# Optimization experiments

Hardware: AMD Instinct MI355X
Metric: run time of the kernel (lower is better)

The kernel has to match this reference:

```python
import jax, jax.numpy as jnp
import numpy as np

# ---- static config (matches init_kwargs) ----
B, N, DIM = 1, 2048, 1024
H, KVH, D = 16, 8, 64
GQ = H // KVH                 # grouped queries per kv head
WS = 64                       # sliding window size (causal, exact)
CBS, STRIDE = 32, 16          # compress block size / sliding stride
SEL_BLK, NSEL, NMEM = 32, 4, 1
NCB = N // STRIDE             # num compressed blocks (128)
NFB = N // SEL_BLK            # num fine blocks (64)
NCPF = SEL_BLK // STRIDE      # compressed blocks per fine block (2)
HID = CBS * D                 # compress MLP hidden (expand factor 1.0)
SCALE = D ** -0.5
THETA = 10000.0
NEG = -jnp.finfo(jnp.float32).max


def setup_inputs():
    key = jax.random.key(0)
    ks = jax.random.split(key, 16)
    s = 0.02
    r = lambda i, shape: jax.random.normal(ks[i], shape, jnp.float32) * s
    return {
        "inp": jax.random.normal(ks[0], (B, N, DIM), jnp.float32),
        "norm_g": jnp.ones((DIM,), jnp.float32),
        "Wqkv": r(1, (DIM, (H + 2 * KVH) * D)),
        "mem_kv": r(2, (2, KVH, NMEM, D)),
        "k_pos": r(3, (KVH, CBS, D)),
        "v_pos": r(4, (KVH, CBS, D)),
        "kW1": r(5, (CBS * D, HID)), "kb1": jnp.zeros((HID,), jnp.float32),
        "kW2": r(6, (HID, D)), "kb2": jnp.zeros((D,), jnp.float32),
        "vW1": r(7, (CBS * D, HID)), "vb1": jnp.zeros((HID,), jnp.float32),
        "vW2": r(8, (HID, D)), "vb2": jnp.zeros((D,), jnp.float32),
        "combW": r(9, (DIM, 3 * H)),
        "combB": jnp.tile(jnp.array([-2.0, -2.0, 2.0], jnp.float32), H),
        "Wout": r(10, (H * D, DIM)),
    }


def _rope(t):
    # lucidrains rotary-embedding-torch: interleaved adjacent-pair rotation
    inv_freq = 1.0 / (THETA ** (jnp.arange(0, D, 2, dtype=jnp.float32) / D))
    ang = jnp.arange(N, dtype=jnp.float32)[:, None] * inv_freq        # [N, D/2]
    cos = jnp.repeat(jnp.cos(ang), 2, axis=-1)                        # [N, D]
    sin = jnp.repeat(jnp.sin(ang), 2, axis=-1)
    t2 = t.reshape(*t.shape[:-1], D // 2, 2)
    rot = jnp.stack([-t2[..., 1], t2[..., 0]], axis=-1).reshape(t.shape)
    return t * cos + rot * sin


def _forward(inp, norm_g, Wqkv, mem_kv, k_pos, v_pos,
             kW1, kb1, kW2, kb2, vW1, vb1, vW2, vb2,
             combW, combB, Wout):
    # RMSNorm
    x = inp * jax.lax.rsqrt(jnp.mean(inp * inp, -1, keepdims=True)
                            + jnp.finfo(inp.dtype).eps) * norm_g
    qkv = x @ Wqkv
    q, k, v = jnp.split(qkv, [H * D, H * D + KVH * D], axis=-1)
    q = q.reshape(B, N, H, D).transpose(0, 2, 1, 3)      # b h n d
    k = k.reshape(B, N, KVH, D).transpose(0, 2, 1, 3)    # b kvh n d
    v = v.reshape(B, N, KVH, D).transpose(0, 2, 1, 3)

    # ---- compressed branch (overlapping windows, left zero pad) ----
    overlap = CBS - STRIDE
    kp = jnp.pad(k, ((0, 0), (0, 0), (overlap, 0), (0, 0)))
    vp = jnp.pad(v, ((0, 0), (0, 0), (overlap, 0), (0, 0)))
    widx = jnp.arange(NCB)[:, None] * STRIDE + jnp.arange(CBS)[None, :]  # [NCB, CBS]
    kw = kp[:, :, widx] + k_pos[None, :, None]   # b kvh w cbs d
    vw = vp[:, :, widx] + v_pos[None, :, None]

    def cmlp(t, W1, b1, W2, b2):
        t = t.reshape(B, KVH, NCB, CBS * D)
        return jax.nn.relu(t @ W1 + b1) @ W2 + b2       # b kvh w d

    ck = cmlp(kw, kW1, kb1, kW2, kb2)
    cv = cmlp(vw, vW1, vb1, vW2, vb2)
    ck = jnp.concatenate([jnp.broadcast_to(mem_kv[0], (B, KVH, NMEM, D)), ck], 2)
    cv = jnp.concatenate([jnp.broadcast_to(mem_kv[1], (B, KVH, NMEM, D)), cv], 2)

    qg = q.reshape(B, KVH, GQ, N, D)
    csim = jnp.einsum('bhgid,bhjd->bhgij', qg, ck) * SCALE   # no mask (cmask=None)
    cattn = jax.nn.softmax(csim, -1)
    cout = jnp.einsum('bhgij,bhjd->bhgid', cattn, cv).reshape(B, H, N, D)

    # rotary AFTER compressed attention (as in source)
    rq, rk = _rope(q), _rope(k)

    # ---- importance scores -> top-k fine block selection ----
    imp = csim[..., NMEM:].mean(2)                          # b kvh n NCB (share grouped q)
    imp = imp.reshape(B, KVH, N, NFB, NCPF).mean(-1)        # mean-pool to fine blocks
    q_blk = jnp.arange(N) // SEL_BLK
    diag = q_blk[:, None] == jnp.arange(NFB)[None, :]
    imp = jnp.where(diag[None, None], NEG, imp)             # mask own (diagonal) block
    imp = jax.nn.softmax(jnp.pad(imp, ((0, 0),) * 3 + ((1, 0),),
                                 constant_values=-1000.0), -1)[..., 1:]
    sel_val, sel_idx = jax.lax.top_k(imp, NSEL)             # b kvh n NSEL

    # ---- fine (block-selected) attention ----
    own = jnp.broadcast_to(q_blk[None, None, :, None], (B, KVH, N, 1))
    sel_idx = jnp.concatenate([sel_idx, own], -1)           # append own block
    fmask = jnp.repeat((sel_val > 1e-10)[..., None], SEL_BLK, -1)  # b kvh n NSEL blk
    causal_row = jnp.tril(jnp.ones((SEL_BLK, SEL_BLK), bool))[jnp.arange(N) % SEL_BLK]
    causal = jnp.broadcast_to(causal_row[None, None, :, None, :],
                              (B, KVH, N, 1, SEL_BLK))
    fmask = jnp.concatenate([fmask, causal], 3).reshape(B, KVH, N, (NSEL + 1) * SEL_BLK)

    fk_blocks = rk.reshape(B, KVH, NFB, SEL_BLK, D)
    fv_blocks = v.reshape(B, KVH, NFB, SEL_BLK, D)
    gather = jax.vmap(jax.vmap(lambda blocks, idx: blocks[idx]))  # over b, kvh
    fk = gather(fk_blocks, sel_idx).reshape(B, KVH, N, (NSEL + 1) * SEL_BLK, D)
    fv = gather(fv_blocks, sel_idx).reshape(B, KVH, N, (NSEL + 1) * SEL_BLK, D)

    rqg = rq.reshape(B, KVH, GQ, N, D)
    fsim = jnp.einsum('bhgid,bhijd->bhgij', rqg, fk) * SCALE
    fsim = jnp.where(fmask[:, :, None], fsim, NEG / 10)
    fattn = jax.nn.softmax(fsim, -1)
    fout = jnp.einsum('bhgij,bhijd->bhgid', fattn, fv).reshape(B, H, N, D)

    # ---- sliding window (causal, exact window size WS) ----
    NW = N // WS
    kp2 = jnp.pad(rk, ((0, 0), (0, 0), (WS, 0), (0, 0)))
    vp2 = jnp.pad(v, ((0, 0), (0, 0), (WS, 0), (0, 0)))
    kidx = jnp.arange(NW)[:, None] * WS + jnp.arange(2 * WS)[None, :]
    kwin = kp2[:, :, kidx]                                  # b kvh nw 2ws d
    vwin = vp2[:, :, kidx]
    qwin = rqg.reshape(B, KVH, GQ, NW, WS, D)
    ssim = jnp.einsum('bhgwid,bhwjd->bhgwij', qwin, kwin) * SCALE
    i = jnp.arange(WS)[:, None]
    j = jnp.arange(2 * WS)[None, :]
    diff = i - (j - WS)
    local_ok = (diff >= 0) & (diff < WS)                    # [WS, 2WS]
    keypos = jnp.arange(NW)[:, None, None] * WS + (jnp.arange(2 * WS) - WS)[None, None, :]
    smask = local_ok[None] & (keypos >= 0)                  # [NW, WS, 2WS]
    ssim = jnp.where(smask[None, None, None], ssim, NEG)
    sattn = jax.nn.softmax(ssim, -1)
    sout = jnp.einsum('bhgwij,bhwjd->bhgwid', sattn, vwin).reshape(B, H, N, D)

    # ---- learned strategy combination (compressed, fine, sliding) ----
    gates = jax.nn.sigmoid(x @ combW + combB).reshape(B, N, H, 3).transpose(0, 2, 1, 3)
    out = gates[..., 0:1] * cout + gates[..., 1:2] * fout + gates[..., 2:3] * sout
    out = out.transpose(0, 2, 1, 3).reshape(B, N, H * D) @ Wout
    return out


def reference(inp, norm_g, Wqkv, mem_kv, k_pos, v_pos,
              kW1, kb1, kW2, kb2, vW1, vb1, vW2, vb2,
              combW, combB, Wout):
    return _forward(inp, norm_g, Wqkv, mem_kv, k_pos, v_pos,
                    kW1, kb1, kW2, kb2, vW1, vb1, vW2, vb2,
                    combW, combB, Wout)
```

## Files before the change

kernel.cpp:

```cpp
#include <hip/hip_runtime.h>
#include <hip/hip_bf16.h>

#define NTOK 2048
#define DIM 1024
#define NH 16
#define KVH 8
#define GQ 2
#define HD 64
#define WS 64
#define CBS 32
#define STRIDE 16
#define SEL_BLK 32
#define NSEL 4
#define NMEM 1
#define NCB 128
#define NFB 64
#define HIDN 2048
#define SCALE 0.125f
#define NEGF (-3.4028234663852886e38f)
#define NEG10F (-3.4028234663852886e37f)

typedef __attribute__((ext_vector_type(8))) short bf16x8;
typedef __attribute__((ext_vector_type(4))) float f32x4;

__device__ __forceinline__ float bflo(unsigned u) { return __uint_as_float(u << 16); }
__device__ __forceinline__ float bfhi(unsigned u) { return __uint_as_float(u & 0xffff0000u); }
__device__ __forceinline__ void dot8(const float4& qa, const float4& qb, uint4 a, float& s) {
    s += qa.x * bflo(a.x) + qa.y * bfhi(a.x) + qa.z * bflo(a.y) + qa.w * bfhi(a.y) +
         qb.x * bflo(a.z) + qb.y * bfhi(a.z) + qb.z * bflo(a.w) + qb.w * bfhi(a.w);
}

__device__ __forceinline__ void gload_lds16(const void* g, void* l) {
    __builtin_amdgcn_global_load_lds((const __attribute__((address_space(1))) unsigned*)g,
                                     (__attribute__((address_space(3))) unsigned*)l, 16, 0, 0);
}

__device__ __forceinline__ void rms_body(const float* __restrict__ inp,
                                         const float* __restrict__ g,
                                         float* __restrict__ x,
                                         __hip_bfloat16* __restrict__ xb, int n) {
    const float* row = inp + (size_t)n * DIM;
    float ss = 0.f;
    for (int c = threadIdx.x; c < DIM; c += 256) { float v = row[c]; ss += v * v; }
    __shared__ float red[4];
    for (int o = 32; o; o >>= 1) ss += __shfl_down(ss, o, 64);
    if ((threadIdx.x & 63) == 0) red[threadIdx.x >> 6] = ss;
    __syncthreads();
    if (threadIdx.x == 0) red[0] = red[0] + red[1] + red[2] + red[3];
    __syncthreads();
    float rs = 1.0f / sqrtf(red[0] / (float)DIM + 1.1920928955078125e-07f);
    float* xr = x + (size_t)n * DIM;
    __hip_bfloat16* xbr = xb + (size_t)n * DIM;
    for (int c = threadIdx.x; c < DIM; c += 256) {
        float v = row[c] * rs * g[c];
        xr[c] = v;
        xbr[c] = __float2bfloat16(v);
    }
}

__device__ __forceinline__ void transpose_body(const float* __restrict__ B,
                                               __hip_bfloat16* __restrict__ Bt,
                                               int K, int N, int bx, int by) {
    __shared__ float tile[32][33];
    int n0 = bx * 32, k0 = by * 32;
    int x = threadIdx.x & 31, y = threadIdx.x >> 5;
    for (int i = 0; i < 4; i++) {
        int k = k0 + y + 8 * i, n = n0 + x;
        tile[y + 8 * i][x] = (k < K && n < N) ? B[(size_t)k * N + n] : 0.f;
    }
    __syncthreads();
    for (int i = 0; i < 4; i++) {
        int n = n0 + y + 8 * i, k = k0 + x;
        if (n < N && k < K) Bt[(size_t)n * K + k] = __float2bfloat16(tile[x][y + 8 * i]);
    }
}

__global__ __launch_bounds__(256) void pre_kernel(
    const float* inp, const float* norm_g, float* x, __hip_bfloat16* xb,
    const float* Wqkv, __hip_bfloat16* Wqkvt,
    const float* kW1, __hip_bfloat16* kW1t,
    const float* vW1, __hip_bfloat16* vW1t,
    const float* Wout, __hip_bfloat16* Woutt,
    const float* combW, __hip_bfloat16* combWt,
    const float* kW2, __hip_bfloat16* kW2t,
    const float* vW2, __hip_bfloat16* vW2t,
    const float* combB, float* gatesb,
    const float* kb2, float* ckraw,
    const float* vb2, float* cvraw) {
    int b = blockIdx.x;
    if (b < 2048) { rms_body(inp, norm_g, x, xb, b); return; }
    b -= 2048;
    if (b < 2048) { transpose_body(Wqkv, Wqkvt, 1024, 2048, b % 64, b / 64); return; }
    b -= 2048;
    if (b < 4096) { transpose_body(kW1, kW1t, 2048, 2048, b % 64, b / 64); return; }
    b -= 4096;
    if (b < 4096) { transpose_body(vW1, vW1t, 2048, 2048, b % 64, b / 64); return; }
    b -= 4096;
    if (b < 1024) { transpose_body(Wout, Woutt, 1024, 1024, b % 32, b / 32); return; }
    b -= 1024;
    if (b < 64) { transpose_body(combW, combWt, 1024, 48, b % 2, b / 2); return; }
    b -= 64;
    if (b < 128) { transpose_body(kW2, kW2t, 2048, 64, b % 2, b / 2); return; }
    b -= 128;
    if (b < 128) { transpose_body(vW2, vW2t, 2048, 64, b % 2, b / 2); return; }
    b -= 128;
    if (b < 384) {
        int idx = b * 256 + threadIdx.x;
        if (idx < 2048 * 48) gatesb[idx] = combB[idx % 48];
        return;
    }
    b -= 384;
    {
        int idx = b * 256 + threadIdx.x;
        int tot = 1024 * 64;
        if (idx < tot) ckraw[idx] = kb2[idx % 64];
        else if (idx < 2 * tot) { idx -= tot; cvraw[idx] = vb2[idx % 64]; }
        return;
    }
}
#define PRE_BLOCKS (2048 + 2048 + 4096 + 4096 + 1024 + 64 + 128 + 128 + 384 + 512)

template <int ACT, int OUTBF16>
__device__ __forceinline__ void mfma_gemm_body(const __hip_bfloat16* __restrict__ A,
                                               const __hip_bfloat16* __restrict__ Bt,
                                               const float* __restrict__ bias,
                                               void* __restrict__ Cp,
                                               int M, int N, int K, int bx, int by) {
    __shared__ __align__(16) short As[128 * 32];
    __shared__ __align__(16) short Bs[128 * 32];
    int tid = threadIdx.x;
    int lane = tid & 63, wave = tid >> 6;
    int wm = (wave >> 1) * 64, wn = (wave & 1) * 64;
    int m0 = by * 128, n0 = bx * 128;
    f32x4 acc[4][4];
    for (int r = 0; r < 4; r++)
        for (int c = 0; c < 4; c++)
            acc[r][c] = (f32x4){0.f, 0.f, 0.f, 0.f};

    int r0 = tid >> 2, kc0 = (tid & 3) * 8;
    int r1 = r0 + 64;

    for (int k0 = 0; k0 < K; k0 += 32) {
        __syncthreads();
        gload_lds16(A + (size_t)(m0 + r0) * K + k0 + kc0, &As[r0 * 32 + kc0]);
        gload_lds16(A + (size_t)(m0 + r1) * K + k0 + kc0, &As[r1 * 32 + kc0]);
        gload_lds16(Bt + (size_t)(n0 + r0) * K + k0 + kc0, &Bs[r0 * 32 + kc0]);
        gload_lds16(Bt + (size_t)(n0 + r1) * K + k0 + kc0, &Bs[r1 * 32 + kc0]);
        __syncthreads();
        bf16x8 af[4], bfr[4];
#pragma unroll
        for (int r = 0; r < 4; r++)
            af[r] = *(const bf16x8*)&As[(wm + r * 16 + (lane & 15)) * 32 + (lane >> 4) * 8];
#pragma unroll
        for (int c = 0; c < 4; c++)
            bfr[c] = *(const bf16x8*)&Bs[(wn + c * 16 + (lane & 15)) * 32 + (lane >> 4) * 8];
#pragma unroll
        for (int r = 0; r < 4; r++)
#pragma unroll
            for (int c = 0; c < 4; c++)
                acc[r][c] = __builtin_amdgcn_mfma_f32_16x16x32_bf16(af[r], bfr[c], acc[r][c], 0, 0, 0);
    }
    for (int r = 0; r < 4; r++) {
        int grow = m0 + wm + r * 16 + (lane >> 4) * 4;
        for (int c = 0; c < 4; c++) {
            int gcol = n0 + wn + c * 16 + (lane & 15);
            float bv = bias ? bias[gcol] : 0.f;
#pragma unroll
            for (int v = 0; v < 4; v++) {
                float val = acc[r][c][v] + bv;
                if (ACT == 1) val = fmaxf(val, 0.f);
                if (OUTBF16)
                    ((__hip_bfloat16*)Cp)[(size_t)(grow + v) * N + gcol] = __float2bfloat16(val);
                else
                    ((float*)Cp)[(size_t)(grow + v) * N + gcol] = val;
            }
        }
    }
}

template <int ACT, int OUTBF16>
__global__ __launch_bounds__(256) void mfma_gemm(const __hip_bfloat16* __restrict__ A,
                                                 const __hip_bfloat16* __restrict__ Bt,
                                                 const float* __restrict__ bias,
                                                 void* __restrict__ Cp,
                                                 int M, int N, int K) {
    mfma_gemm_body<ACT, OUTBF16>(A, Bt, bias, Cp, M, N, K, blockIdx.x, blockIdx.y);
}

__global__ __launch_bounds__(256) void mfma_gemm_pair(const __hip_bfloat16* A0,
                                                      const __hip_bfloat16* A1,
                                                      const __hip_bfloat16* Bt0,
                                                      const __hip_bfloat16* Bt1,
                                                      const float* bias0, const float* bias1,
                                                      __hip_bfloat16* C0, __hip_bfloat16* C1,
                                                      int M, int N, int K) {
    if (blockIdx.z == 0)
        mfma_gemm_body<1, 1>(A0, Bt0, bias0, C0, M, N, K, blockIdx.x, blockIdx.y);
    else
        mfma_gemm_body<1, 1>(A1, Bt1, bias1, C1, M, N, K, blockIdx.x, blockIdx.y);
}

__device__ __forceinline__ void skgemm_body(const __hip_bfloat16* __restrict__ A,
                                            const __hip_bfloat16* __restrict__ Bt,
                                            float* __restrict__ C,
                                            int M, int Nout, int K, int by, int bz, int nz) {
    __shared__ __align__(16) short As2[128 * 32];
    __shared__ __align__(16) short Bs2[64 * 32];
    int tid = threadIdx.x;
    int lane = tid & 63, wave = tid >> 6;
    int m0 = by * 128;
    int wm = wave * 32;
    int kchunk = K / nz;
    int kbase = bz * kchunk;
    f32x4 acc[2][4];
    for (int r = 0; r < 2; r++)
        for (int c = 0; c < 4; c++) acc[r][c] = (f32x4){0.f, 0.f, 0.f, 0.f};

    int ra = tid >> 2, kc = (tid & 3) * 8;
    int rb = ra < Nout ? ra : Nout - 1;
    for (int k0 = kbase; k0 < kbase + kchunk; k0 += 32) {
        __syncthreads();
        gload_lds16(A + (size_t)(m0 + ra) * K + k0 + kc, &As2[ra * 32 + kc]);
        gload_lds16(A + (size_t)(m0 + ra + 64) * K + k0 + kc, &As2[(ra + 64) * 32 + kc]);
        gload_lds16(Bt + (size_t)rb * K + k0 + kc, &Bs2[ra * 32 + kc]);
        __syncthreads();
        bf16x8 af[2], bfr[4];
#pragma unroll
        for (int r = 0; r < 2; r++)
            af[r] = *(const bf16x8*)&As2[(wm + r * 16 + (lane & 15)) * 32 + (lane >> 4) * 8];
#pragma unroll
        for (int c = 0; c < 4; c++)
            bfr[c] = *(const bf16x8*)&Bs2[(c * 16 + (lane & 15)) * 32 + (lane >> 4) * 8];
#pragma unroll
        for (int r = 0; r < 2; r++)
#pragma unroll
            for (int c = 0; c < 4; c++)
                acc[r][c] = __builtin_amdgcn_mfma_f32_16x16x32_bf16(af[r], bfr[c], acc[r][c], 0, 0, 0);
    }
    for (int r = 0; r < 2; r++) {
        int grow = m0 + wm + r * 16 + (lane >> 4) * 4;
        for (int c = 0; c < 4; c++) {
            int gcol = c * 16 + (lane & 15);
            if (gcol >= Nout) continue;
#pragma unroll
            for (int v = 0; v < 4; v++)
                atomicAdd(&C[(size_t)(grow + v) * Nout + gcol], acc[r][c][v]);
        }
    }
}

__global__ __launch_bounds__(256) void qkv_gates_kernel(const __hip_bfloat16* xb,
                                                        const __hip_bfloat16* Wqkvt,
                                                        float* qkv,
                                                        const __hip_bfloat16* combWt,
                                                        float* gatesb) {
    int b = blockIdx.x;
    if (b < 256) {
        mfma_gemm_body<0, 0>(xb, Wqkvt, nullptr, qkv, 2048, 2048, 1024, b & 15, b >> 4);
    } else {
        int s = b - 256;
        skgemm_body(xb, combWt, gatesb, 2048, 48, 1024, s & 15, s >> 4, 4);
    }
}

__global__ __launch_bounds__(256) void skgemm_pair(const __hip_bfloat16* A0,
                                                   const __hip_bfloat16* A1,
                                                   const __hip_bfloat16* Bt0,
                                                   const __hip_bfloat16* Bt1,
                                                   float* C0, float* C1,
                                                   int M, int Nout, int K) {
    if (blockIdx.x == 0)
        skgemm_body(A0, Bt0, C0, M, Nout, K, blockIdx.y, blockIdx.z, gridDim.z);
    else
        skgemm_body(A1, Bt1, C1, M, Nout, K, blockIdx.y, blockIdx.z, gridDim.z);
}

__global__ __launch_bounds__(256) void winrope_kernel(const float* __restrict__ qkv,
                                                      const float* __restrict__ k_pos,
                                                      const float* __restrict__ v_pos,
                                                      __hip_bfloat16* __restrict__ kwflat,
                                                      __hip_bfloat16* __restrict__ vwflat,
                                                      float* __restrict__ rq,
                                                      __hip_bfloat16* __restrict__ rk,
                                                      __hip_bfloat16* __restrict__ vt) {
    int b = blockIdx.x;
    int t = threadIdx.x;
    if (b < 4096) {
        size_t total = (size_t)(KVH * NCB) * HIDN;
        for (size_t e = (size_t)b * 256 + t; e < total; e += (size_t)4096 * 256) {
            int r = (int)(e >> 11);
            int c = (int)(e & 2047);
            int j = c >> 6, d = c & 63;
            int h = r >> 7, i = r & 127;
            int p = i * STRIDE + j - (CBS - STRIDE);
            float kb = k_pos[((size_t)h * CBS + j) * HD + d];
            float vb = v_pos[((size_t)h * CBS + j) * HD + d];
            float kv = 0.f, vv = 0.f;
            if (p >= 0) {
                kv = qkv[(size_t)p * 2048 + 1024 + h * HD + d];
                vv = qkv[(size_t)p * 2048 + 1536 + h * HD + d];
            }
            kwflat[e] = __float2bfloat16(kv + kb);
            vwflat[e] = __float2bfloat16(vv + vb);
        }
        return;
    }
    int n = b - 4096;
    for (int idx = t; idx < NH * 32; idx += 256) {
        int h = idx >> 5, f = idx & 31;
        float inv = exp2f((float)f * -0.41524101186092f);
        float ang = (float)n * inv;
        float cc = cosf(ang), ssn = sinf(ang);
        float a = qkv[(size_t)n * 2048 + h * HD + 2 * f];
        float bq = qkv[(size_t)n * 2048 + h * HD + 2 * f + 1];
        float* o = rq + ((size_t)h * NTOK + n) * HD + 2 * f;
        o[0] = a * cc - bq * ssn;
        o[1] = bq * cc + a * ssn;
    }
    for (int idx = t; idx < KVH * 32; idx += 256) {
        int h = idx >> 5, f = idx & 31;
        float inv = exp2f((float)f * -0.41524101186092f);
        float ang = (float)n * inv;
        float cc = cosf(ang), ssn = sinf(ang);
        float a = qkv[(size_t)n * 2048 + 1024 + h * HD + 2 * f];
        float bq = qkv[(size_t)n * 2048 + 1024 + h * HD + 2 * f + 1];
        __hip_bfloat16* o = rk + ((size_t)h * NTOK + n) * HD + 2 * f;
        o[0] = __float2bfloat16(a * cc - bq * ssn);
        o[1] = __float2bfloat16(bq * cc + a * ssn);
    }
    for (int idx = t; idx < KVH * HD; idx += 256) {
        int h = idx >> 6, d = idx & 63;
        vt[((size_t)h * NTOK + n) * HD + d] =
            __float2bfloat16(qkv[(size_t)n * 2048 + 1536 + h * HD + d]);
    }
}

__global__ __launch_bounds__(256) void cattn2_kernel(const float* __restrict__ qkv,
                                                     const float* __restrict__ ckraw,
                                                     const float* __restrict__ cvraw,
                                                     const float* __restrict__ memkv,
                                                     float* __restrict__ cout,
                                                     int* __restrict__ selidx,
                                                     int* __restrict__ selmask) {
    int h = blockIdx.x >> 6;
    int i0 = (blockIdx.x & 63) * 32;
    int t = threadIdx.x;
    __shared__ float qs[64][68];
    __shared__ float sc[64][132];
    __shared__ float scratch[32 * 68];
    __shared__ float memk[64], memv[64];

    for (int idx = t; idx < 4096; idx += 256) {
        int row = idx >> 6, d = idx & 63;
        int g = row >> 5, qi = row & 31;
        qs[row][d] = qkv[(size_t)(i0 + qi) * 2048 + (h * 2 + g) * 64 + d];
    }
    if (t < 64) { memk[t] = memkv[h * 64 + t]; memv[t] = memkv[(8 + h) * 64 + t]; }
    __syncthreads();
    if (t < 64) {
        float s = 0.f;
        for (int d = 0; d < 64; d++) s += qs[t][d] * memk[d];
        sc[t][0] = s * SCALE;
    }
    int rg = t >> 3, kg = t & 7;
    for (int c = 0; c < 4; c++) {
        __syncthreads();
        for (int idx = t; idx < 2048; idx += 256) {
            int jj = idx >> 6, d = idx & 63;
            scratch[jj * 68 + d] = ckraw[((size_t)h * 128 + c * 32 + jj) * 64 + d];
        }
        __syncthreads();
        float a0[4] = {}, a1[4] = {};
        for (int d = 0; d < 64; d += 4) {
            float4 q0 = *(const float4*)&qs[rg * 2][d];
            float4 q1 = *(const float4*)&qs[rg * 2 + 1][d];
#pragma unroll
            for (int kk = 0; kk < 4; kk++) {
                float4 kv = *(const float4*)&scratch[(kg + kk * 8) * 68 + d];
                a0[kk] += q0.x * kv.x + q0.y * kv.y + q0.z * kv.z + q0.w * kv.w;
                a1[kk] += q1.x * kv.x + q1.y * kv.y + q1.z * kv.z + q1.w * kv.w;
            }
        }
#pragma unroll
        for (int kk = 0; kk < 4; kk++) {
            sc[rg * 2][1 + c * 32 + kg + kk * 8] = a0[kk] * SCALE;
            sc[rg * 2 + 1][1 + c * 32 + kg + kk * 8] = a1[kk] * SCALE;
        }
    }
    __syncthreads();
    for (int idx = t; idx < 2048; idx += 256) {
        int qi = idx >> 6, fb = idx & 63;
        float v = 0.25f * (sc[qi][1 + 2 * fb] + sc[qi][2 + 2 * fb] +
                           sc[32 + qi][1 + 2 * fb] + sc[32 + qi][2 + 2 * fb]);
        if (fb == ((i0 + qi) >> 5)) v = NEGF;
        scratch[qi * 66 + fb] = v;
    }
    __syncthreads();
    if (t < 32) {
        float* row = &scratch[t * 66];
        float m = -1000.f;
        for (int j = 0; j < 64; j++) m = fmaxf(m, row[j]);
        float den = __expf(-1000.f - m);
        for (int j = 0; j < 64; j++) den += __expf(row[j] - m);
        float invd = 1.f / den;
        unsigned long long taken = 0ull;
        int mk = 0;
        size_t base = ((size_t)h * NTOK + i0 + t) * 5;
        for (int p = 0; p < NSEL; p++) {
            float bv = NEGF;
            int bi = 0;
            for (int j = 0; j < 64; j++) {
                if (!((taken >> j) & 1ull) && row[j] > bv) { bv = row[j]; bi = j; }
            }
            taken |= 1ull << bi;
            selidx[base + p] = bi;
            if (__expf(bv - m) * invd > 1e-10f) mk |= 1 << p;
        }
        selidx[base + 4] = (i0 + t) >> 5;
        selmask[h * NTOK + i0 + t] = mk;
    } else if (t >= 64 && t < 128) {
        int r = t - 64;
        float m = NEGF;
        for (int j = 0; j < 129; j++) m = fmaxf(m, sc[r][j]);
        float den = 0.f;
        for (int j = 0; j < 129; j++) { float e = __expf(sc[r][j] - m); sc[r][j] = e; den += e; }
        float inv = 1.f / den;
        for (int j = 0; j < 129; j++) sc[r][j] *= inv;
    }
    __syncthreads();
    int dg = t & 7;
    float o0[8], o1[8];
    {
        float p0 = sc[rg * 2][0], p1 = sc[rg * 2 + 1][0];
#pragma unroll
        for (int dd = 0; dd < 8; dd++) {
            float v = memv[dg + dd * 8];
            o0[dd] = p0 * v;
            o1[dd] = p1 * v;
        }
    }
    for (int c = 0; c < 4; c++) {
        __syncthreads();
        for (int idx = t; idx < 2048; idx += 256) {
            int jj = idx >> 6, d = idx & 63;
            scratch[jj * 68 + d] = cvraw[((size_t)h * 128 + c * 32 + jj) * 64 + d];
        }
        __syncthreads();
        for (int jj = 0; jj < 32; jj++) {
            float p0 = sc[rg * 2][1 + c * 32 + jj];
            float p1 = sc[rg * 2 + 1][1 + c * 32 + jj];
#pragma unroll
            for (int dd = 0; dd < 8; dd++) {
                float v = scratch[jj * 68 + dg + dd * 8];
                o0[dd] += p0 * v;
                o1[dd] += p1 * v;
            }
        }
    }
    {
        int row = rg * 2;
        int g = row >> 5, qi = row & 31;
        int g2 = (row + 1) >> 5, qi2 = (row + 1) & 31;
#pragma unroll
        for (int dd = 0; dd < 8; dd++) {
            cout[(((size_t)(h * 2 + g)) * NTOK + i0 + qi) * 64 + dd * 8 + dg] = o0[dd];
            cout[(((size_t)(h * 2 + g2)) * NTOK + i0 + qi2) * 64 + dd * 8 + dg] = o1[dd];
        }
    }
}

__global__ __launch_bounds__(256) void attn_fused3_kernel(const float* __restrict__ rq,
                                                          const __hip_bfloat16* __restrict__ rk,
                                                          const __hip_bfloat16* __restrict__ vt,
                                                          const int* __restrict__ selidx,
                                                          const int* __restrict__ selmask,
                                                          float* __restrict__ fout,
                                                          float* __restrict__ sout) {
    int tid = threadIdx.x;
    int ws = tid >> 6, lane = tid & 63;
    __shared__ float pbuf[4][448];
    float* pf0 = pbuf[ws];
    float* pf1 = pf0 + 160;
    float* ps0 = pf0 + 320;
    float* ps1 = pf0 + 384;

    int kq = lane >> 2, c = lane & 3;
    int kv8 = lane >> 3, c8 = lane & 7;
    int wid = blockIdx.x * 4 + ws;
    int h = wid >> 11, i = wid & 2047;

    size_t sbase = ((size_t)h * NTOK + i) * 5;
    int selr[5];
#pragma unroll
    for (int s = 0; s < 5; s++) selr[s] = selidx[sbase + s];
    int mk = selmask[h * NTOK + i];

    const float* q0p = rq + ((size_t)(h * 2 + 0) * NTOK + i) * 64 + c * 16;
    const float* q1p = rq + ((size_t)(h * 2 + 1) * NTOK + i) * 64 + c * 16;
    float4 q0[4], q1[4];
#pragma unroll
    for (int u = 0; u < 4; u++) {
        q0[u] = *(const float4*)(q0p + u * 4);
        q1[u] = *(const float4*)(q1p + u * 4);
    }
    int iq = i & 31;

#pragma unroll
    for (int kt = 0; kt < 10; kt++) {
        int slot = kt >> 1;
        int blk = selr[slot];
        int key = kt * 16 + kq;
        int jj = key & 31;
        int kpos = blk * 32 + jj;
        bool valid = (slot < 4) ? (((mk >> slot) & 1) != 0) : (jj <= iq);
        const __hip_bfloat16* kr = rk + ((size_t)h * NTOK + kpos) * 64 + c * 16;
        float s0 = 0.f, s1 = 0.f;
        uint4 a = *(const uint4*)(kr);
        uint4 b = *(const uint4*)(kr + 8);
        dot8(q0[0], q0[1], a, s0); dot8(q0[2], q0[3], b, s0);
        dot8(q1[0], q1[1], a, s1); dot8(q1[2], q1[3], b, s1);
        s0 += __shfl_xor(s0, 1); s0 += __shfl_xor(s0, 2);
        s1 += __shfl_xor(s1, 1); s1 += __shfl_xor(s1, 2);
        if (c == 0) {
            pf0[key] = valid ? s0 * SCALE : NEG10F;
            pf1[key] = valid ? s1 * SCALE : NEG10F;
        }
    }
#pragma unroll
    for (int kt = 0; kt < 4; kt++) {
        int koff = kt * 16 + kq;
        int kpos = i - 63 + koff;
        bool valid = kpos >= 0;
        int kcl = valid ? kpos : 0;
        const __hip_bfloat16* kr = rk + ((size_t)h * NTOK + kcl) * 64 + c * 16;
        float s0 = 0.f, s1 = 0.f;
        uint4 a = *(const uint4*)(kr);
        uint4 b = *(const uint4*)(kr + 8);
        dot8(q0[0], q0[1], a, s0); dot8(q0[2], q0[3], b, s0);
        dot8(q1[0], q1[1], a, s1); dot8(q1[2], q1[3], b, s1);
        s0 += __shfl_xor(s0, 1); s0 += __shfl_xor(s0, 2);
        s1 += __shfl_xor(s1, 1); s1 += __shfl_xor(s1, 2);
        if (c == 0) {
            ps0[koff] = valid ? s0 * SCALE : NEG10F;
            ps1[koff] = valid ? s1 * SCALE : NEG10F;
        }
    }
    {
        float a0 = pf0[lane], b0 = pf0[lane + 64];
        float c0 = (lane < 32) ? pf0[lane + 128] : NEG10F;
        float a1 = pf1[lane], b1 = pf1[lane + 64];
        float c1 = (lane < 32) ? pf1[lane + 128] : NEG10F;
        float m0 = fmaxf(fmaxf(a0, b0), c0);
        float m1 = fmaxf(fmaxf(a1, b1), c1);
#pragma unroll
        for (int o = 1; o < 64; o <<= 1) {
            m0 = fmaxf(m0, __shfl_xor(m0, o));
            m1 = fmaxf(m1, __shfl_xor(m1, o));
        }
        float ea0 = __expf(a0 - m0), eb0 = __expf(b0 - m0), ec0 = (lane < 32) ? __expf(c0 - m0) : 0.f;
        float ea1 = __expf(a1 - m1), eb1 = __expf(b1 - m1), ec1 = (lane < 32) ? __expf(c1 - m1) : 0.f;
        float d0 = ea0 + eb0 + ec0;
        float d1 = ea1 + eb1 + ec1;
#pragma unroll
        for (int o = 1; o < 64; o <<= 1) {
            d0 += __shfl_xor(d0, o);
            d1 += __shfl_xor(d1, o);
        }
        float inv0 = 1.f / d0, inv1 = 1.f / d1;
        pf0[lane] = ea0 * inv0; pf0[lane + 64] = eb0 * inv0;
        pf1[lane] = ea1 * inv1; pf1[lane + 64] = eb1 * inv1;
        if (lane < 32) { pf0[lane + 128] = ec0 * inv0; pf1[lane + 128] = ec1 * inv1; }
    }
    {
        float a0 = ps0[lane], a1 = ps1[lane];
        float m0 = a0, m1 = a1;
#pragma unroll
        for (int o = 1; o < 64; o <<= 1) {
            m0 = fmaxf(m0, __shfl_xor(m0, o));
            m1 = fmaxf(m1, __shfl_xor(m1, o));
        }
        float e0 = __expf(a0 - m0), e1 = __expf(a1 - m1);
        float d0 = e0, d1 = e1;
#pragma unroll
        for (int o = 1; o < 64; o <<= 1) {
            d0 += __shfl_xor(d0, o);
            d1 += __shfl_xor(d1, o);
        }
        ps0[lane] = e0 / d0;
        ps1[lane] = e1 / d1;
    }
    {
        float o0[8] = {}, o1[8] = {};
#pragma unroll
        for (int slot = 0; slot < 5; slot++) {
            const __hip_bfloat16* vbase = vt + ((size_t)h * NTOK + selr[slot] * 32) * 64;
#pragma unroll
            for (int pass = 0; pass < 4; pass++) {
                int j = pass * 8 + kv8;
                uint4 v = *(const uint4*)(vbase + j * 64 + c8 * 8);
                float pa = pf0[slot * 32 + j], pb = pf1[slot * 32 + j];
                float e0 = bflo(v.x), e1 = bfhi(v.x), e2 = bflo(v.y), e3 = bfhi(v.y);
                float e4 = bflo(v.z), e5 = bfhi(v.z), e6 = bflo(v.w), e7 = bfhi(v.w);
                o0[0] = fmaf(pa, e0, o0[0]); o0[1] = fmaf(pa, e1, o0[1]);
                o0[2] = fmaf(pa, e2, o0[2]); o0[3] = fmaf(pa, e3, o0[3]);
                o0[4] = fmaf(pa, e4, o0[4]); o0[5] = fmaf(pa, e5, o0[5]);
                o0[6] = fmaf(pa, e6, o0[6]); o0[7] = fmaf(pa, e7, o0[7]);
                o1[0] = fmaf(pb, e0, o1[0]); o1[1] = fmaf(pb, e1, o1[1]);
                o1[2] = fmaf(pb, e2, o1[2]); o1[3] = fmaf(pb, e3, o1[3]);
                o1[4] = fmaf(pb, e4, o1[4]); o1[5] = fmaf(pb, e5, o1[5]);
                o1[6] = fmaf(pb, e6, o1[6]); o1[7] = fmaf(pb, e7, o1[7]);
            }
        }
#pragma unroll
        for (int o = 8; o <= 32; o <<= 1)
#pragma unroll
            for (int d = 0; d < 8; d++) {
                o0[d] += __shfl_xor(o0[d], o);
                o1[d] += __shfl_xor(o1[d], o);
            }
        if (kv8 == 0) {
            float* f0 = fout + ((size_t)(h * 2 + 0) * NTOK + i) * 64 + c8 * 8;
            float* f1 = fout + ((size_t)(h * 2 + 1) * NTOK + i) * 64 + c8 * 8;
            *(float4*)(f0) = (float4){o0[0], o0[1], o0[2], o0[3]};
            *(float4*)(f0 + 4) = (float4){o0[4], o0[5], o0[6], o0[7]};
            *(float4*)(f1) = (float4){o1[0], o1[1], o1[2], o1[3]};
            *(float4*)(f1 + 4) = (float4){o1[4], o1[5], o1[6], o1[7]};
        }
    }
    {
        float o0[8] = {}, o1[8] = {};
#pragma unroll
        for (int pass = 0; pass < 8; pass++) {
            int j = pass * 8 + kv8;
            int kpos = i - 63 + j;
            int kcl = kpos >= 0 ? kpos : 0;
            uint4 v = *(const uint4*)(vt + ((size_t)h * NTOK + kcl) * 64 + c8 * 8);
            float pa = ps0[j], pb = ps1[j];
            float e0 = bflo(v.x), e1 = bfhi(v.x), e2 = bflo(v.y), e3 = bfhi(v.y);
            float e4 = bflo(v.z), e5 = bfhi(v.z), e6 = bflo(v.w), e7 = bfhi(v.w);
            o0[0] = fmaf(pa, e0, o0[0]); o0[1] = fmaf(pa, e1, o0[1]);
            o0[2] = fmaf(pa, e2, o0[2]); o0[3] = fmaf(pa, e3, o0[3]);
            o0[4] = fmaf(pa, e4, o0[4]); o0[5] = fmaf(pa, e5, o0[5]);
            o0[6] = fmaf(pa, e6, o0[6]); o0[7] = fmaf(pa, e7, o0[7]);
            o1[0] = fmaf(pb, e0, o1[0]); o1[1] = fmaf(pb, e1, o1[1]);
            o1[2] = fmaf(pb, e2, o1[2]); o1[3] = fmaf(pb, e3, o1[3]);
            o1[4] = fmaf(pb, e4, o1[4]); o1[5] = fmaf(pb, e5, o1[5]);
            o1[6] = fmaf(pb, e6, o1[6]); o1[7] = fmaf(pb, e7, o1[7]);
        }
#pragma unroll
        for (int o = 8; o <= 32; o <<= 1)
#pragma unroll
            for (int d = 0; d < 8; d++) {
                o0[d] += __shfl_xor(o0[d], o);
                o1[d] += __shfl_xor(o1[d], o);
            }
        if (kv8 == 0) {
            float* s0p = sout + ((size_t)(h * 2 + 0) * NTOK + i) * 64 + c8 * 8;
            float* s1p = sout + ((size_t)(h * 2 + 1) * NTOK + i) * 64 + c8 * 8;
            *(float4*)(s0p) = (float4){o0[0], o0[1], o0[2], o0[3]};
            *(float4*)(s0p + 4) = (float4){o0[4], o0[5], o0[6], o0[7]};
            *(float4*)(s1p) = (float4){o1[0], o1[1], o1[2], o1[3]};
            *(float4*)(s1p + 4) = (float4){o1[4], o1[5], o1[6], o1[7]};
        }
    }
}

__global__ __launch_bounds__(256) void combine_kernel(const float* __restrict__ gateslin,
                                                      const float* __restrict__ cout,
                                                      const float* __restrict__ fout,
                                                      const float* __restrict__ sout,
                                                      __hip_bfloat16* __restrict__ att) {
    int n = blockIdx.x;
    for (int c = threadIdx.x; c < NH * HD; c += 256) {
        int hd = c >> 6, d = c & 63;
        float g0 = 1.f / (1.f + expf(-gateslin[(size_t)n * (NH * 3) + hd * 3 + 0]));
        float g1 = 1.f / (1.f + expf(-gateslin[(size_t)n * (NH * 3) + hd * 3 + 1]));
        float g2 = 1.f / (1.f + expf(-gateslin[(size_t)n * (NH * 3) + hd * 3 + 2]));
        size_t o = ((size_t)hd * NTOK + n) * HD + d;
        att[(size_t)n * (NH * HD) + c] =
            __float2bfloat16(g0 * cout[o] + g1 * fout[o] + g2 * sout[o]);
    }
}

extern "C" void kernel_launch(void* const* d_in, const int* in_sizes, int n_in,
                              void* d_out, int out_size, void* d_ws, size_t ws_size,
                              hipStream_t stream) {
    const float* inp    = (const float*)d_in[0];
    const float* norm_g = (const float*)d_in[1];
    const float* Wqkv   = (const float*)d_in[2];
    const float* mem_kv = (const float*)d_in[3];
    const float* k_pos  = (const float*)d_in[4];
    const float* v_pos  = (const float*)d_in[5];
    const float* kW1    = (const float*)d_in[6];
    const float* kb1    = (const float*)d_in[7];
    const float* kW2    = (const float*)d_in[8];
    const float* kb2    = (const float*)d_in[9];
    const float* vW1    = (const float*)d_in[10];
    const float* vb1    = (const float*)d_in[11];
    const float* vW2    = (const float*)d_in[12];
    const float* vb2    = (const float*)d_in[13];
    const float* combW  = (const float*)d_in[14];
    const float* combB  = (const float*)d_in[15];
    const float* Wout   = (const float*)d_in[16];
    float* out = (float*)d_out;

    char* base = (char*)d_ws;
    size_t off = 0;
    auto alloc = [&](size_t bytes) {
        void* p = base + off;
        off += (bytes + 255) & ~(size_t)255;
        return p;
    };
    float* x            = (float*)alloc((size_t)NTOK * DIM * 4);
    __hip_bfloat16* xb  = (__hip_bfloat16*)alloc((size_t)NTOK * DIM * 2);
    float* qkv          = (float*)alloc((size_t)NTOK * 2048 * 4);
    __hip_bfloat16* Wqkvt = (__hip_bfloat16*)alloc((size_t)2048 * 1024 * 2);
    __hip_bfloat16* kW1t  = (__hip_bfloat16*)alloc((size_t)2048 * 2048 * 2);
    __hip_bfloat16* vW1t  = (__hip_bfloat16*)alloc((size_t)2048 * 2048 * 2);
    __hip_bfloat16* Woutt = (__hip_bfloat16*)alloc((size_t)1024 * 1024 * 2);
    __hip_bfloat16* combWt = (__hip_bfloat16*)alloc((size_t)48 * 1024 * 2);
    __hip_bfloat16* kW2t  = (__hip_bfloat16*)alloc((size_t)64 * 2048 * 2);
    __hip_bfloat16* vW2t  = (__hip_bfloat16*)alloc((size_t)64 * 2048 * 2);
    __hip_bfloat16* kwflat = (__hip_bfloat16*)alloc((size_t)KVH * NCB * HIDN * 2);
    __hip_bfloat16* vwflat = (__hip_bfloat16*)alloc((size_t)KVH * NCB * HIDN * 2);
    __hip_bfloat16* hidkb = (__hip_bfloat16*)alloc((size_t)KVH * NCB * HIDN * 2);
    __hip_bfloat16* hidvb = (__hip_bfloat16*)alloc((size_t)KVH * NCB * HIDN * 2);
    float* ckraw        = (float*)alloc((size_t)KVH * NCB * HD * 4);
    float* cvraw        = (float*)alloc((size_t)KVH * NCB * HD * 4);
    float* rq           = (float*)alloc((size_t)NH * NTOK * HD * 4);
    __hip_bfloat16* rk  = (__hip_bfloat16*)alloc((size_t)KVH * NTOK * HD * 2);
    __hip_bfloat16* vt  = (__hip_bfloat16*)alloc((size_t)KVH * NTOK * HD * 2);
    float* coutb        = (float*)alloc((size_t)NH * NTOK * HD * 4);
    float* foutb        = (float*)alloc((size_t)NH * NTOK * HD * 4);
    float* soutb        = (float*)alloc((size_t)NH * NTOK * HD * 4);
    float* gatesb       = (float*)alloc((size_t)NTOK * NH * 3 * 4);
    __hip_bfloat16* attb = (__hip_bfloat16*)alloc((size_t)NTOK * DIM * 2);
    int* selidx         = (int*)alloc((size_t)KVH * NTOK * 5 * 4);
    int* selmask        = (int*)alloc((size_t)KVH * NTOK * 4);
    (void)ws_size; (void)in_sizes; (void)n_in; (void)out_size;

    pre_kernel<<<PRE_BLOCKS, 256, 0, stream>>>(inp, norm_g, x, xb,
                                               Wqkv, Wqkvt, kW1, kW1t, vW1, vW1t,
                                               Wout, Woutt, combW, combWt,
                                               kW2, kW2t, vW2, vW2t,
                                               combB, gatesb, kb2, ckraw, vb2, cvraw);
    qkv_gates_kernel<<<320, 256, 0, stream>>>(xb, Wqkvt, qkv, combWt, gatesb);
    winrope_kernel<<<4096 + 2048, 256, 0, stream>>>(qkv, k_pos, v_pos, kwflat, vwflat,
                                                    rq, rk, vt);
    mfma_gemm_pair<<<dim3(16, 8, 2), 256, 0, stream>>>(kwflat, vwflat, kW1t, vW1t,
                                                       kb1, vb1, hidkb, hidvb,
                                                       1024, 2048, 2048);
    skgemm_pair<<<dim3(2, 8, 8), 256, 0, stream>>>(hidkb, hidvb, kW2t, vW2t,
                                                   ckraw, cvraw, 1024, 64, 2048);
    cattn2_kernel<<<KVH * (NTOK / 32), 256, 0, stream>>>(qkv, ckraw, cvraw, mem_kv,
                                                         coutb, selidx, selmask);
    attn_fused3_kernel<<<4096, 256, 0, stream>>>(rq, rk, vt, selidx, selmask,
                                                 foutb, soutb);
    combine_kernel<<<NTOK, 256, 0, stream>>>(gatesb, coutb, foutb, soutb, attb);
    mfma_gemm<0, 0><<<dim3(8, 16), 256, 0, stream>>>(attb, Woutt, nullptr, out, 2048, 1024, 1024);
}
```

Baseline: 382.5 us.

## Split sliding-window attention into LDS-tiled blocks sharing K/V across queries

The fused attention kernel now launches two kinds of blocks. Sliding-window blocks stage a 79-row K/V window for 16 consecutive queries of one head into LDS and compute all of them from shared memory. Fine-selection blocks keep the previous per-query global-load path. This removes the redundant global K/V reads each query made for its 64-key window, at the cost of more LDS per block, a __syncthreads, and a serial loop of four queries per wave.

```diff
diff --git a/kernel.cpp b/kernel.cpp
--- a/kernel.cpp
+++ b/kernel.cpp
@@ -469,7 +469,11 @@
     }
 }
 
-__global__ __launch_bounds__(256) void attn_fused3_kernel(const float* __restrict__ rq,
+#define SLIDE_BLKS 1024
+#define SROWS 79
+#define SPAD 72
+#define SLIDE_LDS (SROWS * SPAD * 2 * 2 + 4 * 128 * 4)
+__global__ __launch_bounds__(256) void attn_fused4_kernel(const float* __restrict__ rq,
                                                           const __hip_bfloat16* __restrict__ rk,
                                                           const __hip_bfloat16* __restrict__ vt,
                                                           const int* __restrict__ selidx,
@@ -478,118 +482,183 @@
                                                           float* __restrict__ sout) {
     int tid = threadIdx.x;
     int ws = tid >> 6, lane = tid & 63;
-    __shared__ float pbuf[4][448];
-    float* pf0 = pbuf[ws];
-    float* pf1 = pf0 + 160;
-    float* ps0 = pf0 + 320;
-    float* ps1 = pf0 + 384;
+    __shared__ __align__(16) char smem[SLIDE_LDS];
 
     int kq = lane >> 2, c = lane & 3;
     int kv8 = lane >> 3, c8 = lane & 7;
-    int wid = blockIdx.x * 4 + ws;
-    int h = wid >> 11, i = wid & 2047;
-
-    size_t sbase = ((size_t)h * NTOK + i) * 5;
-    int selr[5];
-#pragma unroll
-    for (int s = 0; s < 5; s++) selr[s] = selidx[sbase + s];
-    int mk = selmask[h * NTOK + i];
-
-    const float* q0p = rq + ((size_t)(h * 2 + 0) * NTOK + i) * 64 + c * 16;
-    const float* q1p = rq + ((size_t)(h * 2 + 1) * NTOK + i) * 64 + c * 16;
-    float4 q0[4], q1[4];
-#pragma unroll
-    for (int u = 0; u < 4; u++) {
-        q0[u] = *(const float4*)(q0p + u * 4);
-        q1[u] = *(const float4*)(q1p + u * 4);
-    }
-    int iq = i & 31;
-
-#pragma unroll
-    for (int kt = 0; kt < 10; kt++) {
-        int slot = kt >> 1;
-        int blk = selr[slot];
-        int key = kt * 16 + kq;
-        int jj = key & 31;
-        int kpos = blk * 32 + jj;
-        bool valid = (slot < 4) ? (((mk >> slot) & 1) != 0) : (jj <= iq);
-        const __hip_bfloat16* kr = rk + ((size_t)h * NTOK + kpos) * 64 + c * 16;
-        float s0 = 0.f, s1 = 0.f;
-        uint4 a = *(const uint4*)(kr);
-        uint4 b = *(const uint4*)(kr + 8);
-        dot8(q0[0], q0[1], a, s0); dot8(q0[2], q0[3], b, s0);
-        dot8(q1[0], q1[1], a, s1); dot8(q1[2], q1[3], b, s1);
-        s0 += __shfl_xor(s0, 1); s0 += __shfl_xor(s0, 2);
-        s1 += __shfl_xor(s1, 1); s1 += __shfl_xor(s1, 2);
-        if (c == 0) {
-            pf0[key] = valid ? s0 * SCALE : NEG10F;
-            pf1[key] = valid ? s1 * SCALE : NEG10F;
-        }
-    }
-#pragma unroll
-    for (int kt = 0; kt < 4; kt++) {
-        int koff = kt * 16 + kq;
-        int kpos = i - 63 + koff;
-        bool valid = kpos >= 0;
-        int kcl = valid ? kpos : 0;
-        const __hip_bfloat16* kr = rk + ((size_t)h * NTOK + kcl) * 64 + c * 16;
-        float s0 = 0.f, s1 = 0.f;
-        uint4 a = *(const uint4*)(kr);
-        uint4 b = *(const uint4*)(kr + 8);
-        dot8(q0[0], q0[1], a, s0); dot8(q0[2], q0[3], b, s0);
-        dot8(q1[0], q1[1], a, s1); dot8(q1[2], q1[3], b, s1);
-        s0 += __shfl_xor(s0, 1); s0 += __shfl_xor(s0, 2);
-        s1 += __shfl_xor(s1, 1); s1 += __shfl_xor(s1, 2);
-        if (c == 0) {
-            ps0[koff] = valid ? s0 * SCALE : NEG10F;
-            ps1[koff] = valid ? s1 * SCALE : NEG10F;
-        }
-    }
-    {
-        float a0 = pf0[lane], b0 = pf0[lane + 64];
-        float c0 = (lane < 32) ? pf0[lane + 128] : NEG10F;
-        float a1 = pf1[lane], b1 = pf1[lane + 64];
-        float c1 = (lane < 32) ? pf1[lane + 128] : NEG10F;
-        float m0 = fmaxf(fmaxf(a0, b0), c0);
-        float m1 = fmaxf(fmaxf(a1, b1), c1);
-#pragma unroll
-        for (int o = 1; o < 64; o <<= 1) {
-            m0 = fmaxf(m0, __shfl_xor(m0, o));
-            m1 = fmaxf(m1, __shfl_xor(m1, o));
-        }
-        float ea0 = __expf(a0 - m0), eb0 = __expf(b0 - m0), ec0 = (lane < 32) ? __expf(c0 - m0) : 0.f;
-        float ea1 = __expf(a1 - m1), eb1 = __expf(b1 - m1), ec1 = (lane < 32) ? __expf(c1 - m1) : 0.f;
-        float d0 = ea0 + eb0 + ec0;
-        float d1 = ea1 + eb1 + ec1;
-#pragma unroll
-        for (int o = 1; o < 64; o <<= 1) {
-            d0 += __shfl_xor(d0, o);
-            d1 += __shfl_xor(d1, o);
-        }
-        float inv0 = 1.f / d0, inv1 = 1.f / d1;
-        pf0[lane] = ea0 * inv0; pf0[lane + 64] = eb0 * inv0;
-        pf1[lane] = ea1 * inv1; pf1[lane + 64] = eb1 * inv1;
-        if (lane < 32) { pf0[lane + 128] = ec0 * inv0; pf1[lane + 128] = ec1 * inv1; }
-    }
-    {
-        float a0 = ps0[lane], a1 = ps1[lane];
-        float m0 = a0, m1 = a1;
-#pragma unroll
-        for (int o = 1; o < 64; o <<= 1) {
-            m0 = fmaxf(m0, __shfl_xor(m0, o));
-            m1 = fmaxf(m1, __shfl_xor(m1, o));
-        }
-        float e0 = __expf(a0 - m0), e1 = __expf(a1 - m1);
-        float d0 = e0, d1 = e1;
-#pragma unroll
-        for (int o = 1; o < 64; o <<= 1) {
-            d0 += __shfl_xor(d0, o);
-            d1 += __shfl_xor(d1, o);
-        }
-        ps0[lane] = e0 / d0;
-        ps1[lane] = e1 / d1;
-    }
-    {
+
+    if (blockIdx.x < SLIDE_BLKS) {
+        int h = blockIdx.x & 7;
+        int q0 = (int)(blockIdx.x >> 3) * 16;
+        short* ks = (short*)smem;
+        short* vs = ks + SROWS * SPAD;
+        float* ps = (float*)(smem + SROWS * SPAD * 2 * 2);
+        int basek = q0 - 63;
+        for (int idx = tid; idx < SROWS * 8; idx += 256) {
+            int row = idx >> 3, ch = (idx & 7) * 8;
+            int kpos = basek + row;
+            uint4 kv = (uint4){0u, 0u, 0u, 0u}, vv = (uint4){0u, 0u, 0u, 0u};
+            if (kpos >= 0) {
+                kv = *(const uint4*)(rk + ((size_t)h * NTOK + kpos) * 64 + ch);
+                vv = *(const uint4*)(vt + ((size_t)h * NTOK + kpos) * 64 + ch);
+            }
+            *(uint4*)&ks[row * SPAD + ch] = kv;
+            *(uint4*)&vs[row * SPAD + ch] = vv;
+        }
+        __syncthreads();
+        float* p0 = ps + ws * 128;
+        float* p1 = p0 + 64;
+#pragma unroll 1
+        for (int tq = 0; tq < 4; tq++) {
+            int ibase = ws * 4 + tq;
+            int i = q0 + ibase;
+            const float* q0p = rq + ((size_t)(h * 2 + 0) * NTOK + i) * 64 + c * 16;
+            const float* q1p = rq + ((size_t)(h * 2 + 1) * NTOK + i) * 64 + c * 16;
+            float4 qa[4], qb[4];
+#pragma unroll
+            for (int u = 0; u < 4; u++) {
+                qa[u] = *(const float4*)(q0p + u * 4);
+                qb[u] = *(const float4*)(q1p + u * 4);
+            }
+#pragma unroll
+            for (int kt = 0; kt < 4; kt++) {
+                int key = kt * 16 + kq;
+                const short* kr = &ks[(ibase + key) * SPAD + c * 16];
+                float s0 = 0.f, s1 = 0.f;
+                uint4 a = *(const uint4*)(kr);
+                uint4 b = *(const uint4*)(kr + 8);
+                dot8(qa[0], qa[1], a, s0); dot8(qa[2], qa[3], b, s0);
+                dot8(qb[0], qb[1], a, s1); dot8(qb[2], qb[3], b, s1);
+                s0 += __shfl_xor(s0, 1); s0 += __shfl_xor(s0, 2);
+                s1 += __shfl_xor(s1, 1); s1 += __shfl_xor(s1, 2);
+                int kpos = i - 63 + key;
+                if (c == 0) {
+                    p0[key] = (kpos >= 0) ? s0 * SCALE : NEG10F;
+                    p1[key] = (kpos >= 0) ? s1 * SCALE : NEG10F;
+                }
+            }
+            {
+                float a0 = p0[lane], a1 = p1[lane];
+                float m0 = a0, m1 = a1;
+#pragma unroll
+                for (int o = 1; o < 64; o <<= 1) {
+                    m0 = fmaxf(m0, __shfl_xor(m0, o));
+                    m1 = fmaxf(m1, __shfl_xor(m1, o));
+                }
+                float e0 = __expf(a0 - m0), e1 = __expf(a1 - m1);
+                float d0 = e0, d1 = e1;
+#pragma unroll
+                for (int o = 1; o < 64; o <<= 1) {
+                    d0 += __shfl_xor(d0, o);
+                    d1 += __shfl_xor(d1, o);
+                }
+                p0[lane] = e0 / d0;
+                p1[lane] = e1 / d1;
+            }
+            float o0[8] = {}, o1[8] = {};
+#pragma unroll
+            for (int pass = 0; pass < 8; pass++) {
+                int j = pass * 8 + kv8;
+                uint4 v = *(const uint4*)&vs[(ibase + j) * SPAD + c8 * 8];
+                float pa = p0[j], pb = p1[j];
+                float e0 = bflo(v.x), e1 = bfhi(v.x), e2 = bflo(v.y), e3 = bfhi(v.y);
+                float e4 = bflo(v.z), e5 = bfhi(v.z), e6 = bflo(v.w), e7 = bfhi(v.w);
+                o0[0] = fmaf(pa, e0, o0[0]); o0[1] = fmaf(pa, e1, o0[1]);
+                o0[2] = fmaf(pa, e2, o0[2]); o0[3] = fmaf(pa, e3, o0[3]);
+                o0[4] = fmaf(pa, e4, o0[4]); o0[5] = fmaf(pa, e5, o0[5]);
+                o0[6] = fmaf(pa, e6, o0[6]); o0[7] = fmaf(pa, e7, o0[7]);
+                o1[0] = fmaf(pb, e0, o1[0]); o1[1] = fmaf(pb, e1, o1[1]);
+                o1[2] = fmaf(pb, e2, o1[2]); o1[3] = fmaf(pb, e3, o1[3]);
+                o1[4] = fmaf(pb, e4, o1[4]); o1[5] = fmaf(pb, e5, o1[5]);
+                o1[6] = fmaf(pb, e6, o1[6]); o1[7] = fmaf(pb, e7, o1[7]);
+            }
+#pragma unroll
+            for (int o = 8; o <= 32; o <<= 1)
+#pragma unroll
+                for (int d = 0; d < 8; d++) {
+                    o0[d] += __shfl_xor(o0[d], o);
+                    o1[d] += __shfl_xor(o1[d], o);
+                }
+            if (kv8 == 0) {
+                float* s0p = sout + ((size_t)(h * 2 + 0) * NTOK + i) * 64 + c8 * 8;
+                float* s1p = sout + ((size_t)(h * 2 + 1) * NTOK + i) * 64 + c8 * 8;
+                *(float4*)(s0p) = (float4){o0[0], o0[1], o0[2], o0[3]};
+                *(float4*)(s0p + 4) = (float4){o0[4], o0[5], o0[6], o0[7]};
+                *(float4*)(s1p) = (float4){o1[0], o1[1], o1[2], o1[3]};
+                *(float4*)(s1p + 4) = (float4){o1[4], o1[5], o1[6], o1[7]};
+            }
+        }
+    } else {
+        int bb = blockIdx.x - SLIDE_BLKS;
+        int h = bb & 7;
+        int i = (bb >> 3) * 4 + ws;
+        float* pbuf = (float*)smem;
+        float* pf0 = pbuf + ws * 320;
+        float* pf1 = pf0 + 160;
+
+        size_t sbase = ((size_t)h * NTOK + i) * 5;
+        int selr[5];
+#pragma unroll
+        for (int s = 0; s < 5; s++) selr[s] = selidx[sbase + s];
+        int mk = selmask[h * NTOK + i];
+
+        const float* q0p = rq + ((size_t)(h * 2 + 0) * NTOK + i) * 64 + c * 16;
+        const float* q1p = rq + ((size_t)(h * 2 + 1) * NTOK + i) * 64 + c * 16;
+        float4 q0[4], q1[4];
+#pragma unroll
+        for (int u = 0; u < 4; u++) {
+            q0[u] = *(const float4*)(q0p + u * 4);
+            q1[u] = *(const float4*)(q1p + u * 4);
+        }
+        int iq = i & 31;
+
+#pragma unroll
+        for (int kt = 0; kt < 10; kt++) {
+            int slot = kt >> 1;
+            int blk = selr[slot];
+            int key = kt * 16 + kq;
+            int jj = key & 31;
+            int kpos = blk * 32 + jj;
+            bool valid = (slot < 4) ? (((mk >> slot) & 1) != 0) : (jj <= iq);
+            const __hip_bfloat16* kr = rk + ((size_t)h * NTOK + kpos) * 64 + c * 16;
+            float s0 = 0.f, s1 = 0.f;
+            uint4 a = *(const uint4*)(kr);
+            uint4 b = *(const uint4*)(kr + 8);
+            dot8(q0[0], q0[1], a, s0); dot8(q0[2], q0[3], b, s0);
+            dot8(q1[0], q1[1], a, s1); dot8(q1[2], q1[3], b, s1);
+            s0 += __shfl_xor(s0, 1); s0 += __shfl_xor(s0, 2);
+            s1 += __shfl_xor(s1, 1); s1 += __shfl_xor(s1, 2);
+            if (c == 0) {
+                pf0[key] = valid ? s0 * SCALE : NEG10F;
+                pf1[key] = valid ? s1 * SCALE : NEG10F;
+            }
+        }
+        {
+            float a0 = pf0[lane], b0 = pf0[lane + 64];
+            float c0 = (lane < 32) ? pf0[lane + 128] : NEG10F;
+            float a1 = pf1[lane], b1 = pf1[lane + 64];
+            float c1 = (lane < 32) ? pf1[lane + 128] : NEG10F;
+            float m0 = fmaxf(fmaxf(a0, b0), c0);
+            float m1 = fmaxf(fmaxf(a1, b1), c1);
+#pragma unroll
+            for (int o = 1; o < 64; o <<= 1) {
+                m0 = fmaxf(m0, __shfl_xor(m0, o));
+                m1 = fmaxf(m1, __shfl_xor(m1, o));
+            }
+            float ea0 = __expf(a0 - m0), eb0 = __expf(b0 - m0), ec0 = (lane < 32) ? __expf(c0 - m0) : 0.f;
+            float ea1 = __expf(a1 - m1), eb1 = __expf(b1 - m1), ec1 = (lane < 32) ? __expf(c1 - m1) : 0.f;
+            float d0 = ea0 + eb0 + ec0;
+            float d1 = ea1 + eb1 + ec1;
+#pragma unroll
+            for (int o = 1; o < 64; o <<= 1) {
+                d0 += __shfl_xor(d0, o);
+                d1 += __shfl_xor(d1, o);
+            }
+            float inv0 = 1.f / d0, inv1 = 1.f / d1;
+            pf0[lane] = ea0 * inv0; pf0[lane + 64] = eb0 * inv0;
+            pf1[lane] = ea1 * inv1; pf1[lane + 64] = eb1 * inv1;
+            if (lane < 32) { pf0[lane + 128] = ec0 * inv0; pf1[lane + 128] = ec1 * inv1; }
+        }
         float o0[8] = {}, o1[8] = {};
 #pragma unroll
         for (int slot = 0; slot < 5; slot++) {
@@ -625,42 +694,6 @@
             *(float4*)(f0 + 4) = (float4){o0[4], o0[5], o0[6], o0[7]};
             *(float4*)(f1) = (float4){o1[0], o1[1], o1[2], o1[3]};
             *(float4*)(f1 + 4) = (float4){o1[4], o1[5], o1[6], o1[7]};
-        }
-    }
-    {
-        float o0[8] = {}, o1[8] = {};
-#pragma unroll
-        for (int pass = 0; pass < 8; pass++) {
-            int j = pass * 8 + kv8;
-            int kpos = i - 63 + j;
-            int kcl = kpos >= 0 ? kpos : 0;
-            uint4 v = *(const uint4*)(vt + ((size_t)h * NTOK + kcl) * 64 + c8 * 8);
-            float pa = ps0[j], pb = ps1[j];
-            float e0 = bflo(v.x), e1 = bfhi(v.x), e2 = bflo(v.y), e3 = bfhi(v.y);
-            float e4 = bflo(v.z), e5 = bfhi(v.z), e6 = bflo(v.w), e7 = bfhi(v.w);
-            o0[0] = fmaf(pa, e0, o0[0]); o0[1] = fmaf(pa, e1, o0[1]);
-            o0[2] = fmaf(pa, e2, o0[2]); o0[3] = fmaf(pa, e3, o0[3]);
-            o0[4] = fmaf(pa, e4, o0[4]); o0[5] = fmaf(pa, e5, o0[5]);
-            o0[6] = fmaf(pa, e6, o0[6]); o0[7] = fmaf(pa, e7, o0[7]);
-            o1[0] = fmaf(pb, e0, o1[0]); o1[1] = fmaf(pb, e1, o1[1]);
-            o1[2] = fmaf(pb, e2, o1[2]); o1[3] = fmaf(pb, e3, o1[3]);
-            o1[4] = fmaf(pb, e4, o1[4]); o1[5] = fmaf(pb, e5, o1[5]);
-            o1[6] = fmaf(pb, e6, o1[6]); o1[7] = fmaf(pb, e7, o1[7]);
-        }
-#pragma unroll
-        for (int o = 8; o <= 32; o <<= 1)
-#pragma unroll
-            for (int d = 0; d < 8; d++) {
-                o0[d] += __shfl_xor(o0[d], o);
-                o1[d] += __shfl_xor(o1[d], o);
-            }
-        if (kv8 == 0) {
-            float* s0p = sout + ((size_t)(h * 2 + 0) * NTOK + i) * 64 + c8 * 8;
-            float* s1p = sout + ((size_t)(h * 2 + 1) * NTOK + i) * 64 + c8 * 8;
-            *(float4*)(s0p) = (float4){o0[0], o0[1], o0[2], o0[3]};
-            *(float4*)(s0p + 4) = (float4){o0[4], o0[5], o0[6], o0[7]};
-            *(float4*)(s1p) = (float4){o1[0], o1[1], o1[2], o1[3]};
-            *(float4*)(s1p + 4) = (float4){o1[4], o1[5], o1[6], o1[7]};
         }
     }
 }
@@ -754,8 +787,8 @@
                                                    ckraw, cvraw, 1024, 64, 2048);
     cattn2_kernel<<<KVH * (NTOK / 32), 256, 0, stream>>>(qkv, ckraw, cvraw, mem_kv,
                                                          coutb, selidx, selmask);
-    attn_fused3_kernel<<<4096, 256, 0, stream>>>(rq, rk, vt, selidx, selmask,
-                                                 foutb, soutb);
+    attn_fused4_kernel<<<SLIDE_BLKS + 4096, 256, 0, stream>>>(rq, rk, vt, selidx, selmask,
+                                                              foutb, soutb);
     combine_kernel<<<NTOK, 256, 0, stream>>>(gatesb, coutb, foutb, soutb, attb);
     mfma_gemm<0, 0><<<dim3(8, 16), 256, 0, stream>>>(attb, Woutt, nullptr, out, 2048, 1024, 1024);
 }
```

After: 371.4 us. -2.9%, faster.
